# Kernel tuning notes

Hardware: AMD Instinct MI355X
Metric: run time of the kernel (lower is better)

Reference implementation:

```python
import math
import jax, jax.numpy as jnp
import numpy as np

B, CIN, COUT, K, Z, H, W = 8, 512, 512, 3, 512, 64, 64


def setup_inputs() -> dict:
    key = jax.random.key(0)
    k1, k2, k3, k4 = jax.random.split(key, 4)
    inp = {
        "input": jax.random.normal(k1, (B, CIN, H, W), dtype=jnp.float32),
        "style": jax.random.normal(k2, (B, Z), dtype=jnp.float32),
        # base conv weight: [1, out, in, k, k]
        "weight": jax.random.normal(k3, (1, COUT, CIN, K, K), dtype=jnp.float32),
        # EqualLinear modulation params (lr_mul=1, bias_init=1)
        "mod_w": jax.random.normal(k4, (CIN, Z), dtype=jnp.float32),
        "mod_b": jnp.ones((CIN,), dtype=jnp.float32),
    }
    return inp


def reference(input, style, weight, mod_w, mod_b):
    # EqualLinear: scale = 1/sqrt(z_dim), lr_mul = 1, no activation
    z_dim = mod_w.shape[1]
    mod_scale = 1.0 / math.sqrt(z_dim)
    s = style @ (mod_w * mod_scale).T + mod_b  # [B, in]

    # modulated per-sample weights: scale * base_weight * style
    in_ch, k = weight.shape[2], weight.shape[-1]
    conv_scale = 1.0 / math.sqrt(in_ch * k * k)
    w = conv_scale * weight * s[:, None, :, None, None]  # [B, out, in, k, k]

    pad = k // 2

    def conv_one(x, wb):  # x: [in, H, W], wb: [out, in, k, k]
        return jax.lax.conv_general_dilated(
            x[None], wb, window_strides=(1, 1),
            padding=[(pad, pad), (pad, pad)],
            dimension_numbers=("NCHW", "OIHW", "NCHW"),
        )[0]

    out = jax.vmap(conv_one)(input, w)  # [B, out, H, W]
    return out
```

## Files before the change

### kernel.cpp

```cpp
#include <hip/hip_runtime.h>
#include <hip/hip_bf16.h>

#define BB   8
#define CIN  512
#define COUT 512
#define ZD   512
#define HH   64
#define WW   64

#define MOD_SCALE  0.04419417382415922f
#define CONV_SCALE 0.014731391274719742f

typedef __bf16 bf16x8 __attribute__((ext_vector_type(8)));
typedef float  f32x4  __attribute__((ext_vector_type(4)));
typedef float  f32x16 __attribute__((ext_vector_type(16)));

static __device__ __forceinline__ unsigned short f32_to_bf16_rne(float f) {
    unsigned int u = __float_as_uint(f);
    u = (u + 0x7FFFu + ((u >> 16) & 1u)) >> 16;
    return (unsigned short)u;
}

__global__ void k_style(const float* __restrict__ style, const float* __restrict__ mod_w,
                        const float* __restrict__ mod_b, float* __restrict__ sconv) {
    int wid  = blockIdx.x * 4 + (threadIdx.x >> 6);
    int lane = threadIdx.x & 63;
    int b = wid >> 9;
    int i = wid & 511;
    const float4* st = (const float4*)(style + (size_t)b * ZD);
    const float4* mw = (const float4*)(mod_w + (size_t)i * ZD);
    float4 a0 = st[lane],      b0 = mw[lane];
    float4 a1 = st[lane + 64], b1 = mw[lane + 64];
    float sum = a0.x*b0.x + a0.y*b0.y + a0.z*b0.z + a0.w*b0.w
              + a1.x*b1.x + a1.y*b1.y + a1.z*b1.z + a1.w*b1.w;
    #pragma unroll
    for (int off = 32; off > 0; off >>= 1) sum += __shfl_down(sum, off);
    if (lane == 0) sconv[wid] = (sum * MOD_SCALE + mod_b[i]) * CONV_SCALE;
}

__global__ void k_zero_border(unsigned short* __restrict__ xs2p) {
    int b = blockIdx.y;
    int p = blockIdx.x * 4 + (threadIdx.x >> 6);
    int lane = threadIdx.x & 63;
    int h, w;
    if (p < 66)       { h = 0;       w = p; }
    else if (p < 132) { h = 65;      w = p - 66; }
    else if (p < 196) { h = p - 131; w = 0; }
    else              { h = p - 195; w = 65; }
    int4 z = {0, 0, 0, 0};
    *(int4*)&xs2p[((size_t)(b * 66 + h) * 66 + w) * 512 + lane * 8] = z;
}

__global__ void k_scale_input(const float* __restrict__ input, const float* __restrict__ sconv,
                              unsigned short* __restrict__ xs2p) {
    int i0 = blockIdx.x * 32;
    int h  = blockIdx.y;
    int b  = blockIdx.z;
    __shared__ unsigned short lds[64][40];
    #pragma unroll
    for (int r = 0; r < 8; ++r) {
        int ii = r * 4 + (threadIdx.x >> 6);
        int w  = threadIdx.x & 63;
        float v = input[(((size_t)b * CIN + i0 + ii) * HH + h) * WW + w];
        float s = sconv[b * CIN + i0 + ii];
        lds[w][ii] = f32_to_bf16_rne(v * s);
    }
    __syncthreads();
    int w = threadIdx.x >> 2, q = threadIdx.x & 3;
    int4 val = *(const int4*)&lds[w][q * 8];
    *(int4*)&xs2p[((size_t)(b * 66 + h + 1) * 66 + (w + 1)) * 512 + i0 + q * 8] = val;
}

__global__ void k_weight(const float* __restrict__ weight, unsigned short* __restrict__ w3) {
    int t = blockIdx.x * 256 + threadIdx.x;
    int o = t >> 9, i = t & 511;
    int c = i >> 5, g = (i >> 3) & 3, il = i & 7;
    int h = o >> 8, ol = o & 255;
    const float* src = weight + ((size_t)o * CIN + i) * 9;
    #pragma unroll
    for (int p = 0; p < 9; ++p) {
        size_t gran = ((size_t)(c * 9 + p) * 2 + h) * 1024 + g * 256 + ol;
        w3[gran * 8 + il] = f32_to_bf16_rne(src[p]);
    }
}

#define GLD(srcp, ldsbyte)                                                        \
    __builtin_amdgcn_global_load_lds(                                             \
        (const __attribute__((address_space(1))) unsigned int*)(srcp),            \
        (__attribute__((address_space(3))) unsigned int*)(smb + (ldsbyte)),       \
        16, 0, 0)

#define MFMA8(Af, Bf)                                                             \
    _Pragma("unroll") for (int mt = 0; mt < 4; ++mt)                              \
        _Pragma("unroll") for (int nt = 0; nt < 2; ++nt)                          \
            acc[mt][nt] = __builtin_amdgcn_mfma_f32_32x32x16_bf16(                \
                Af[mt], Bf[nt], acc[mt][nt], 0, 0, 0);

#define TAP(t, Nmid, DOX, DOW, LASTTS) {                                          \
    const int kh0 = (t) / 3, kw0 = (t) % 3;                                       \
    const int tn  = ((t) + 1) % 9;                                                \
    const int kh1 = tn / 3, kw1 = tn % 3;                                         \
    const int wnx = (wrd + 16384) & 65535;                                        \
    const int wwr = (wrd + 49152) & 65535;                                        \
    const int xrdn = ((t) == 8) ? (xrd ^ 32768) : xrd;                            \
                                  \
    if ((DOX) && (t) == 0) GLD(sxn +  0, xwr + 0 * 8192 + wdst);                  \
    if ((DOX) && (t) == 1) GLD(sxn + 32, xwr + 2 * 8192 + wdst);                  \
    if (DOW) GLD(pW, wwr + wdst);                                                 \
    {   const char* wb = smb + wrd + 8192 + aoff;                                 \
        const char* xb = smb + xrd + 16384 + boff + kh0 * 1056 + kw0 * 16;        \
        aB[0] = *(const bf16x8*)(wb);        aB[1] = *(const bf16x8*)(wb + 512);  \
        aB[2] = *(const bf16x8*)(wb + 1024); aB[3] = *(const bf16x8*)(wb + 1536); \
        bB[0] = *(const bf16x8*)(xb);        bB[1] = *(const bf16x8*)(xb + 512);  \
    }                                                                             \
    __builtin_amdgcn_s_setprio(1);                                                \
    MFMA8(aA, bA)                                                                 \
    __builtin_amdgcn_s_setprio(0);                                                \
    asm volatile("s_waitcnt vmcnt(" #Nmid ")" ::: "memory");                      \
    __builtin_amdgcn_s_barrier();                                                 \
                                  \
    if ((DOX) && (t) == 0) GLD(sxn + 16, xwr + 1 * 8192 + wdst);                  \
    if ((DOX) && (t) == 1) GLD(sxn + 48, xwr + 3 * 8192 + wdst);                  \
    if (DOW) { GLD(pW + 8192, wwr + 8192 + wdst); pW += 32768; }                  \
    if (!(LASTTS)) {                                                              \
        const char* wb = smb + wnx + aoff;                                        \
        const char* xb = smb + xrdn + boff + kh1 * 1056 + kw1 * 16;               \
        aA[0] = *(const bf16x8*)(wb);        aA[1] = *(const bf16x8*)(wb + 512);  \
        aA[2] = *(const bf16x8*)(wb + 1024); aA[3] = *(const bf16x8*)(wb + 1536); \
        bA[0] = *(const bf16x8*)(xb);        bA[1] = *(const bf16x8*)(xb + 512);  \
    }                                                                             \
    __builtin_amdgcn_s_setprio(1);                                                \
    MFMA8(aB, bB)                                                                 \
    __builtin_amdgcn_s_setprio(0);                                                \
    __builtin_amdgcn_s_barrier();                                                 \
    wrd = wnx;                                                                    \
}

__global__ __launch_bounds__(512, 2)
void k_conv(const unsigned short* __restrict__ xs2p, const unsigned short* __restrict__ w3,
            float* __restrict__ out) {
    __shared__ unsigned short smem[65536];
    char* smb = (char*)smem;

    const int tid  = threadIdx.x;
    const int wid  = tid >> 6, lane = tid & 63;
    const int wm   = wid >> 2, wr   = wid & 3;
    const int l31  = lane & 31, l5  = lane >> 5;
    const int half = blockIdx.x;
    const int oc0  = half * 256;
    const int y0   = blockIdx.y * 4;
    const int b    = blockIdx.z;

    const int p_lin = wid * 64 + lane;
    const int xrow  = p_lin / 66;
    const int xcol  = p_lin - xrow * 66;
    const char* srcX = (const char*)xs2p;
    if (p_lin < 396)
        srcX += ((size_t)(b * 66 + y0 + xrow) * 66 + xcol) * 1024;

    const char* pW0 = (const char*)w3 + (size_t)half * 16384 + p_lin * 16;
    const int wdst = p_lin * 16;

    GLD(srcX +  0, 65536 + 0 * 8192 + wdst);
    GLD(srcX + 16, 65536 + 1 * 8192 + wdst);
    GLD(srcX + 32, 65536 + 2 * 8192 + wdst);
    GLD(srcX + 48, 65536 + 3 * 8192 + wdst);
    GLD(pW0,          0     + wdst);
    GLD(pW0 +  8192,  8192  + wdst);
    GLD(pW0 + 32768,  16384 + wdst);
    GLD(pW0 + 40960,  24576 + wdst);
    GLD(pW0 + 65536,  32768 + wdst);
    GLD(pW0 + 73728,  40960 + wdst);
    const char* pW = pW0 + 3 * 32768;
    asm volatile("s_waitcnt vmcnt(4)" ::: "memory");
    __builtin_amdgcn_s_barrier();

    f32x16 acc[4][2];
    #pragma unroll
    for (int mt = 0; mt < 4; ++mt)
        #pragma unroll
        for (int nt = 0; nt < 2; ++nt)
            acc[mt][nt] = (f32x16)(0.f);

    const int aoff = l5 * 4096 + (wm * 128 + l31) * 16;
    const int boff = l5 * 8192 + (wr * 66 + l31) * 16;

    bf16x8 aA[4], bA[2], aB[4], bB[2];
    int wrd = 0;
    int xrd = 65536;
    const char* sxn = srcX + 64;

    {
        const char* wb = smb + aoff;
        const char* xb = smb + 65536 + boff;
        aA[0] = *(const bf16x8*)(wb);        aA[1] = *(const bf16x8*)(wb + 512);
        aA[2] = *(const bf16x8*)(wb + 1024); aA[3] = *(const bf16x8*)(wb + 1536);
        bA[0] = *(const bf16x8*)(xb);        bA[1] = *(const bf16x8*)(xb + 512);
    }

    for (int c = 0; c < 15; ++c) {
        const int xwr = xrd ^ 32768;
        TAP(0, 4, 1, 1, 0) TAP(1, 6, 1, 1, 0) TAP(2, 5, 0, 1, 0)
        TAP(3, 3, 0, 1, 0) TAP(4, 3, 0, 1, 0) TAP(5, 3, 0, 1, 0)
        TAP(6, 3, 0, 1, 0) TAP(7, 3, 0, 1, 0) TAP(8, 3, 0, 1, 0)
        sxn += 64; xrd ^= 32768;
    }
    {
        const int xwr = 0; (void)xwr;
        TAP(0, 3, 0, 1, 0) TAP(1, 3, 0, 1, 0) TAP(2, 3, 0, 1, 0)
        TAP(3, 3, 0, 1, 0) TAP(4, 3, 0, 1, 0) TAP(5, 3, 0, 1, 0)
        TAP(6, 2, 0, 0, 0) TAP(7, 0, 0, 0, 0) TAP(8, 0, 0, 0, 1)
    }

    const int ybase = (y0 + wr) * 64;
    #pragma unroll
    for (int mt = 0; mt < 4; ++mt)
        #pragma unroll
        for (int nt = 0; nt < 2; ++nt)
            #pragma unroll
            for (int r = 0; r < 16; ++r) {
                int row = (r & 3) + 8 * (r >> 2) + 4 * l5;
                int oc  = oc0 + wm * 128 + mt * 32 + row;
                out[((size_t)(b * COUT + oc) << 12) + ybase + nt * 32 + l31] = acc[mt][nt][r];
            }
}

extern "C" void kernel_launch(void* const* d_in, const int* in_sizes, int n_in,
                              void* d_out, int out_size, void* d_ws, size_t ws_size,
                              hipStream_t stream) {
    const float* input  = (const float*)d_in[0];
    const float* style  = (const float*)d_in[1];
    const float* weight = (const float*)d_in[2];
    const float* mod_w  = (const float*)d_in[3];
    const float* mod_b  = (const float*)d_in[4];
    float* out = (float*)d_out;

    const size_t xs2p_bytes = (size_t)BB * 66 * 66 * 512 * 2;
    const size_t w3_bytes   = (size_t)144 * 2 * 1024 * 8 * 2;
    const size_t need = 16384 + xs2p_bytes + w3_bytes;
    if (ws_size < need) return;

    float*          sconv = (float*)d_ws;
    unsigned short* xs2p  = (unsigned short*)((char*)d_ws + 16384);
    unsigned short* w3    = (unsigned short*)((char*)d_ws + 16384 + xs2p_bytes);

    hipLaunchKernelGGL(k_style,       dim3(1024),      dim3(256), 0, stream, style, mod_w, mod_b, sconv);
    hipLaunchKernelGGL(k_weight,      dim3(1024),      dim3(256), 0, stream, weight, w3);
    hipLaunchKernelGGL(k_zero_border, dim3(65, 8),     dim3(256), 0, stream, xs2p);
    hipLaunchKernelGGL(k_scale_input, dim3(16, 64, 8), dim3(256), 0, stream, input, sconv, xs2p);
    hipLaunchKernelGGL(k_conv,        dim3(2, 16, 8),  dim3(512), 0, stream, xs2p, w3, out);
}
```

Baseline: 165.9 us.

## Replace split-phase register ping-pong with single-barrier per-tap load-then-MFMA schedule

Restructures each tap so all LDS fragment reads for both K-halves are issued up front, followed by one barrier, a full lgkmcnt wait, and 16 back-to-back MFMAs. The old scheme interleaved half the MFMAs with prefetching the next tap's fragments across two barriers. The intent is to halve the barriers per tap and give the MFMA stream an uninterrupted block. The cost is that LDS read latency is no longer hidden behind the previous MFMAs within a wave, so it relies on the second resident block per CU to cover the gap. The global-load issue order and vmcnt thresholds are adjusted to match.

Measured after the change: 164.1 us. No clear change (-1.0%).

```diff
diff --git a/kernel.cpp b/kernel.cpp
--- a/kernel.cpp
+++ b/kernel.cpp
@@ -90,50 +90,40 @@
         (__attribute__((address_space(3))) unsigned int*)(smb + (ldsbyte)),       \
         16, 0, 0)
 
-#define MFMA8(Af, Bf)                                                             \
+#define TAP(t, VMA, DOX, DOW) {                                                   \
+    const int kh_ = (t) / 3, kw_ = (t) % 3;                                       \
+    const int wwr_ = (wrd + 49152) & 65535;                                       \
+    if (DOW) { GLD(pW, wwr_ + wdst); GLD(pW + 8192, wwr_ + 8192 + wdst);          \
+               pW += 32768; }                                                     \
+    if ((DOX) && (t) == 0) { GLD(sxn +  0, xwr + 0 * 8192 + wdst);                \
+                             GLD(sxn + 16, xwr + 1 * 8192 + wdst); }              \
+    if ((DOX) && (t) == 1) { GLD(sxn + 32, xwr + 2 * 8192 + wdst);                \
+                             GLD(sxn + 48, xwr + 3 * 8192 + wdst); }              \
+    {   const char* wb = smb + wrd + aoff;                                        \
+        const char* xb = smb + xrd + boff + kh_ * 1056 + kw_ * 16;                \
+        aA[0] = *(const bf16x8*)(wb);        aA[1] = *(const bf16x8*)(wb + 512);  \
+        aA[2] = *(const bf16x8*)(wb + 1024); aA[3] = *(const bf16x8*)(wb + 1536); \
+        aB[0] = *(const bf16x8*)(wb + 8192);        aB[1] = *(const bf16x8*)(wb + 8704);  \
+        aB[2] = *(const bf16x8*)(wb + 9216);        aB[3] = *(const bf16x8*)(wb + 9728);  \
+        bA[0] = *(const bf16x8*)(xb);        bA[1] = *(const bf16x8*)(xb + 512);  \
+        bB[0] = *(const bf16x8*)(xb + 16384); bB[1] = *(const bf16x8*)(xb + 16896); \
+    }                                                                             \
+    asm volatile("s_waitcnt vmcnt(" #VMA ")" ::: "memory");                       \
+    __builtin_amdgcn_s_barrier();                                                 \
+    asm volatile("s_waitcnt lgkmcnt(0)");                                         \
+    __builtin_amdgcn_sched_barrier(0);                                            \
+    __builtin_amdgcn_s_setprio(1);                                                \
     _Pragma("unroll") for (int mt = 0; mt < 4; ++mt)                              \
         _Pragma("unroll") for (int nt = 0; nt < 2; ++nt)                          \
             acc[mt][nt] = __builtin_amdgcn_mfma_f32_32x32x16_bf16(                \
-                Af[mt], Bf[nt], acc[mt][nt], 0, 0, 0);
-
-#define TAP(t, Nmid, DOX, DOW, LASTTS) {                                          \
-    const int kh0 = (t) / 3, kw0 = (t) % 3;                                       \
-    const int tn  = ((t) + 1) % 9;                                                \
-    const int kh1 = tn / 3, kw1 = tn % 3;                                         \
-    const int wnx = (wrd + 16384) & 65535;                                        \
-    const int wwr = (wrd + 49152) & 65535;                                        \
-    const int xrdn = ((t) == 8) ? (xrd ^ 32768) : xrd;                            \
-                                  \
-    if ((DOX) && (t) == 0) GLD(sxn +  0, xwr + 0 * 8192 + wdst);                  \
-    if ((DOX) && (t) == 1) GLD(sxn + 32, xwr + 2 * 8192 + wdst);                  \
-    if (DOW) GLD(pW, wwr + wdst);                                                 \
-    {   const char* wb = smb + wrd + 8192 + aoff;                                 \
-        const char* xb = smb + xrd + 16384 + boff + kh0 * 1056 + kw0 * 16;        \
-        aB[0] = *(const bf16x8*)(wb);        aB[1] = *(const bf16x8*)(wb + 512);  \
-        aB[2] = *(const bf16x8*)(wb + 1024); aB[3] = *(const bf16x8*)(wb + 1536); \
-        bB[0] = *(const bf16x8*)(xb);        bB[1] = *(const bf16x8*)(xb + 512);  \
-    }                                                                             \
-    __builtin_amdgcn_s_setprio(1);                                                \
-    MFMA8(aA, bA)                                                                 \
-    __builtin_amdgcn_s_setprio(0);                                                \
-    asm volatile("s_waitcnt vmcnt(" #Nmid ")" ::: "memory");                      \
-    __builtin_amdgcn_s_barrier();                                                 \
-                                  \
-    if ((DOX) && (t) == 0) GLD(sxn + 16, xwr + 1 * 8192 + wdst);                  \
-    if ((DOX) && (t) == 1) GLD(sxn + 48, xwr + 3 * 8192 + wdst);                  \
-    if (DOW) { GLD(pW + 8192, wwr + 8192 + wdst); pW += 32768; }                  \
-    if (!(LASTTS)) {                                                              \
-        const char* wb = smb + wnx + aoff;                                        \
-        const char* xb = smb + xrdn + boff + kh1 * 1056 + kw1 * 16;               \
-        aA[0] = *(const bf16x8*)(wb);        aA[1] = *(const bf16x8*)(wb + 512);  \
-        aA[2] = *(const bf16x8*)(wb + 1024); aA[3] = *(const bf16x8*)(wb + 1536); \
-        bA[0] = *(const bf16x8*)(xb);        bA[1] = *(const bf16x8*)(xb + 512);  \
-    }                                                                             \
-    __builtin_amdgcn_s_setprio(1);                                                \
-    MFMA8(aB, bB)                                                                 \
+                aA[mt], bA[nt], acc[mt][nt], 0, 0, 0);                            \
+    _Pragma("unroll") for (int mt = 0; mt < 4; ++mt)                              \
+        _Pragma("unroll") for (int nt = 0; nt < 2; ++nt)                          \
+            acc[mt][nt] = __builtin_amdgcn_mfma_f32_32x32x16_bf16(                \
+                aB[mt], bB[nt], acc[mt][nt], 0, 0, 0);                            \
     __builtin_amdgcn_s_setprio(0);                                                \
     __builtin_amdgcn_s_barrier();                                                 \
-    wrd = wnx;                                                                    \
+    wrd = (wrd + 16384) & 65535;                                                  \
 }
 
 __global__ __launch_bounds__(512, 2)
@@ -185,31 +175,23 @@
     const int aoff = l5 * 4096 + (wm * 128 + l31) * 16;
     const int boff = l5 * 8192 + (wr * 66 + l31) * 16;
 
-    bf16x8 aA[4], bA[2], aB[4], bB[2];
+    bf16x8 aA[4], aB[4], bA[2], bB[2];
     int wrd = 0;
     int xrd = 65536;
     const char* sxn = srcX + 64;
 
-    {
-        const char* wb = smb + aoff;
-        const char* xb = smb + 65536 + boff;
-        aA[0] = *(const bf16x8*)(wb);        aA[1] = *(const bf16x8*)(wb + 512);
-        aA[2] = *(const bf16x8*)(wb + 1024); aA[3] = *(const bf16x8*)(wb + 1536);
-        bA[0] = *(const bf16x8*)(xb);        bA[1] = *(const bf16x8*)(xb + 512);
-    }
-
     for (int c = 0; c < 15; ++c) {
         const int xwr = xrd ^ 32768;
-        TAP(0, 4, 1, 1, 0) TAP(1, 6, 1, 1, 0) TAP(2, 5, 0, 1, 0)
-        TAP(3, 3, 0, 1, 0) TAP(4, 3, 0, 1, 0) TAP(5, 3, 0, 1, 0)
-        TAP(6, 3, 0, 1, 0) TAP(7, 3, 0, 1, 0) TAP(8, 3, 0, 1, 0)
+        TAP(0, 6, 1, 1) TAP(1, 8, 1, 1) TAP(2, 8, 0, 1)
+        TAP(3, 6, 0, 1) TAP(4, 4, 0, 1) TAP(5, 4, 0, 1)
+        TAP(6, 4, 0, 1) TAP(7, 4, 0, 1) TAP(8, 4, 0, 1)
         sxn += 64; xrd ^= 32768;
     }
     {
         const int xwr = 0; (void)xwr;
-        TAP(0, 3, 0, 1, 0) TAP(1, 3, 0, 1, 0) TAP(2, 3, 0, 1, 0)
-        TAP(3, 3, 0, 1, 0) TAP(4, 3, 0, 1, 0) TAP(5, 3, 0, 1, 0)
-        TAP(6, 2, 0, 0, 0) TAP(7, 0, 0, 0, 0) TAP(8, 0, 0, 0, 1)
+        TAP(0, 4, 0, 1) TAP(1, 4, 0, 1) TAP(2, 4, 0, 1)
+        TAP(3, 4, 0, 1) TAP(4, 4, 0, 1) TAP(5, 4, 0, 1)
+        TAP(6, 2, 0, 0) TAP(7, 0, 0, 0) TAP(8, 0, 0, 0)
     }
 
     const int ybase = (y0 + wr) * 64;
```
